# Kernel optimization log

Hardware: AMD Instinct MI355X
Metric: run time of the kernel (lower is better)

## Reference

```python
import jax, jax.numpy as jnp
import numpy as np
import math

B, T, C, H = 8, 1024, 1024, 16
D = C // H  # head_size = 64
FF = 4 * C


def setup_inputs() -> dict:
    key = jax.random.key(0)
    ks = jax.random.split(key, 8)
    s = 0.02
    return {
        "x": jax.random.normal(ks[0], (B, T, C), jnp.float32),
        "ln1_g": jnp.ones((C,), jnp.float32),
        "ln1_b": jnp.zeros((C,), jnp.float32),
        "attn_w": jax.random.normal(ks[1], (C, 3 * C), jnp.float32) * s,
        "attn_b": jnp.zeros((3 * C,), jnp.float32),
        "attn_proj_w": jax.random.normal(ks[2], (C, C), jnp.float32) * s,
        "attn_proj_b": jnp.zeros((C,), jnp.float32),
        "ln2_g": jnp.ones((C,), jnp.float32),
        "ln2_b": jnp.zeros((C,), jnp.float32),
        "fc_w": jax.random.normal(ks[3], (C, FF), jnp.float32) * s,
        "fc_b": jnp.zeros((FF,), jnp.float32),
        "mlp_proj_w": jax.random.normal(ks[4], (FF, C), jnp.float32) * s,
        "mlp_proj_b": jnp.zeros((C,), jnp.float32),
    }


def _layernorm(x, g, b, eps=1e-5):
    mu = jnp.mean(x, axis=-1, keepdims=True)
    var = jnp.mean(jnp.square(x - mu), axis=-1, keepdims=True)
    return (x - mu) * jax.lax.rsqrt(var + eps) * g + b


def reference(x, ln1_g, ln1_b, attn_w, attn_b, attn_proj_w, attn_proj_b,
              ln2_g, ln2_b, fc_w, fc_b, mlp_proj_w, mlp_proj_b):
    # --- attention branch (pre-LN) ---
    h = _layernorm(x, ln1_g, ln1_b)
    kqv = h @ attn_w + attn_b                      # (B,T,3C)
    # NOTE: source splits as k, q, v (k first!)
    k, q, v = jnp.split(kqv, 3, axis=-1)
    k = k.reshape(B, T, H, D).transpose(0, 2, 1, 3)  # (B,H,T,D)
    q = q.reshape(B, T, H, D).transpose(0, 2, 1, 3)
    v = v.reshape(B, T, H, D).transpose(0, 2, 1, 3)
    # NOTE: source computes k @ q^T, i.e. wei[i,j] = k_i . q_j
    scale = 1.0 / math.sqrt(D)
    wei = jnp.einsum('bhid,bhjd->bhij', k, q) * scale  # (B,H,T,T)
    causal = jnp.tril(jnp.ones((T, T), dtype=bool))
    wei = jnp.where(causal, wei, -jnp.inf)
    wei = jax.nn.softmax(wei, axis=-1)
    out = jnp.einsum('bhij,bhjd->bhid', wei, v)        # (B,H,T,D)
    out = out.transpose(0, 2, 1, 3).reshape(B, T, C)
    out = out @ attn_proj_w + attn_proj_b
    x = x + out
    # --- MLP branch (pre-LN) ---
    h2 = _layernorm(x, ln2_g, ln2_b)
    m = jax.nn.gelu(h2 @ fc_w + fc_b, approximate=False)  # torch GELU default = exact erf
    m = m @ mlp_proj_w + mlp_proj_b
    return x + m
```

## Files before the change

kernel.cpp:

```cpp
#include <hip/hip_runtime.h>
#include <stdint.h>

typedef unsigned short u16;
typedef __bf16 bf16x8 __attribute__((ext_vector_type(8)));
typedef float f32x4 __attribute__((ext_vector_type(4)));

#define DEVINL static __device__ __forceinline__

DEVINL u16 f2bf(float f) {
  uint32_t u = __builtin_bit_cast(uint32_t, f);
  u += 0x7fffu + ((u >> 16) & 1u);
  return (u16)(u >> 16);
}

DEVINL uint32_t pack_bf2(float f0, float f1) {
  uint32_t u0 = __builtin_bit_cast(uint32_t, f0) + 0x8000u;
  uint32_t u1 = __builtin_bit_cast(uint32_t, f1) + 0x8000u;
  return __builtin_amdgcn_perm(u1, u0, 0x07060302u);
}

DEVINL bf16x8 ld_frag(const u16* p) { return *(const bf16x8*)p; }

DEVINL void gld_lds16(const void* g, void* l) {
  __builtin_amdgcn_global_load_lds((const __attribute__((address_space(1))) void*)g,
                                   (__attribute__((address_space(3))) void*)l, 16, 0, 0);
}

DEVINL int swz4(int r) { return (r & 3) ^ ((r >> 2) & 3); }

DEVINL void xcd_tile(int& tm, int& tn) {
  const int gx = gridDim.x;
  const int flat = blockIdx.x + gx * blockIdx.y;
  const int q = (gx * gridDim.y) >> 3;
  const int wg = (flat & 7) * q + (flat >> 3);
  tn = (wg % gx) * 128;
  tm = (wg / gx) * 128;
}

__global__ __launch_bounds__(256)
void transpose_bf16(const float* __restrict__ W, u16* __restrict__ Wt, int K, int N) {
  __shared__ float tile[32][33];
  const int n0 = blockIdx.x * 32, k0 = blockIdx.y * 32;
  const int tx = threadIdx.x, ty = threadIdx.y;
#pragma unroll
  for (int i = 0; i < 32; i += 8)
    tile[ty + i][tx] = W[(size_t)(k0 + ty + i) * N + n0 + tx];
  __syncthreads();
#pragma unroll
  for (int i = 0; i < 32; i += 8)
    Wt[(size_t)(n0 + ty + i) * K + k0 + tx] = f2bf(tile[tx][ty + i]);
}

__global__ __launch_bounds__(256)
void ln_kernel(const float* __restrict__ x, const float* __restrict__ g,
               const float* __restrict__ b, u16* __restrict__ out) {
  __shared__ float red[8];
  const size_t row = blockIdx.x;
  const int tid = threadIdx.x;
  float4 v = ((const float4*)(x + row * 1024))[tid];
  float s = v.x + v.y + v.z + v.w;
  float s2 = v.x * v.x + v.y * v.y + v.z * v.z + v.w * v.w;
#pragma unroll
  for (int o = 32; o; o >>= 1) { s += __shfl_down(s, o); s2 += __shfl_down(s2, o); }
  const int w = tid >> 6;
  if ((tid & 63) == 0) { red[w * 2] = s; red[w * 2 + 1] = s2; }
  __syncthreads();
  const float S = red[0] + red[2] + red[4] + red[6];
  const float S2 = red[1] + red[3] + red[5] + red[7];
  const float mu = S * (1.f / 1024.f);
  const float var = S2 * (1.f / 1024.f) - mu * mu;
  const float rstd = rsqrtf(var + 1e-5f);
  float4 gv = ((const float4*)g)[tid];
  float4 bv = ((const float4*)b)[tid];
  ushort4 o;
  o.x = f2bf((v.x - mu) * rstd * gv.x + bv.x);
  o.y = f2bf((v.y - mu) * rstd * gv.y + bv.y);
  o.z = f2bf((v.z - mu) * rstd * gv.z + bv.z);
  o.w = f2bf((v.w - mu) * rstd * gv.w + bv.w);
  ((ushort4*)(out + row * 1024))[tid] = o;
}

enum { EPI_KQV = 0, EPI_RESID = 1, EPI_GELU = 2, EPI_ADD = 3 };

template <int EPI>
DEVINL void gemm_epilogue(f32x4 (&acc)[4][4], const float* __restrict__ bias,
                          void* __restrict__ outp, const float* __restrict__ resid,
                          int N, int tm, int tn, int mh, int nh, int q4, int c) {
#pragma unroll
  for (int mt = 0; mt < 4; ++mt) {
#pragma unroll
    for (int nt = 0; nt < 4; ++nt) {
      const int col = tn + nh + nt * 16 + c;
      const float bcol = bias[col];
#pragma unroll
      for (int rg = 0; rg < 4; ++rg) {
        const int row = tm + mh + mt * 16 + q4 * 4 + rg;
        float val = acc[mt][nt][rg] + bcol;
        if constexpr (EPI == EPI_KQV) {
          const int bb = row >> 10, t = row & 1023;
          const int s = col >> 10, rem = col & 1023;
          const int hh = rem >> 6, d = rem & 63;
          if (s == 0) val *= 0.18033688011112042f;
          const size_t base = ((size_t)((bb * 16 + hh) * 3 + s)) << 16;
          const size_t idx = (s == 2) ? base + (size_t)d * 1024 + t : base + (size_t)t * 64 + d;
          ((u16*)outp)[idx] = f2bf(val);
        } else if constexpr (EPI == EPI_RESID) {
          const size_t idx = (size_t)row * 1024 + col;
          ((float*)outp)[idx] = val + resid[idx];
        } else if constexpr (EPI == EPI_GELU) {
          const float x2 = val * val;
          const float t = __builtin_fmaf(x2, -0.102952445f, -2.30221235f);
          const float e = __builtin_amdgcn_exp2f(val * t);
          const float ge = val * __builtin_amdgcn_rcpf(1.0f + e);
          ((u16*)outp)[(size_t)row * N + col] = f2bf(ge);
        } else {
          const size_t idx = (size_t)row * 1024 + col;
          ((float*)outp)[idx] += val;
        }
      }
    }
  }
}

template <int EPI>
DEVINL void gemm_body2(const u16* __restrict__ A, const u16* __restrict__ Bt,
                       const float* __restrict__ bias, void* __restrict__ outp,
                       const float* __restrict__ resid, int M, int N, int K,
                       int tm, int tn) {
  __shared__ alignas(16) u16 sA[2][128 * 32];
  __shared__ alignas(16) u16 sB[2][128 * 32];
  const int tid = threadIdx.x;
  const int w = tid >> 6, l = tid & 63;
  const int q4 = l >> 4, c = l & 15;
  const int mh = (w >> 1) * 64, nh = (w & 1) * 64;
  const int cg8 = (q4 ^ swz4(c)) * 8;

  f32x4 acc[4][4] = {};

  const int srow = l >> 2;
  const int scol = ((l & 3) ^ swz4(srow)) * 8;
  const u16* gA0 = A + (size_t)(tm + (w * 2) * 16 + srow) * K + scol;
  const u16* gA1 = A + (size_t)(tm + (w * 2 + 1) * 16 + srow) * K + scol;
  const u16* gB0 = Bt + (size_t)(tn + (w * 2) * 16 + srow) * K + scol;
  const u16* gB1 = Bt + (size_t)(tn + (w * 2 + 1) * 16 + srow) * K + scol;
  const int cA0 = (w * 2) * 512, cA1 = (w * 2 + 1) * 512;

  const int nIters = K / 32;
#define STAGE2(buf, k0)                         \
  do {                                          \
    gld_lds16(gA0 + (k0), &sA[buf][cA0]);       \
    gld_lds16(gA1 + (k0), &sA[buf][cA1]);       \
    gld_lds16(gB0 + (k0), &sB[buf][cA0]);       \
    gld_lds16(gB1 + (k0), &sB[buf][cA1]);       \
  } while (0)

  STAGE2(0, 0);
  for (int i = 0; i < nIters; ++i) {
    const int cur = i & 1;
    asm volatile("s_waitcnt vmcnt(0)" ::: "memory");
    __syncthreads();
    if (i + 1 < nIters) STAGE2(cur ^ 1, (i + 1) * 32);
    const u16* bA = sA[cur];
    const u16* bB = sB[cur];
    bf16x8 af[4], bfv[4];
#pragma unroll
    for (int mt = 0; mt < 4; ++mt) af[mt] = ld_frag(bA + (mh + mt * 16 + c) * 32 + cg8);
#pragma unroll
    for (int nt = 0; nt < 4; ++nt) bfv[nt] = ld_frag(bB + (nh + nt * 16 + c) * 32 + cg8);
#pragma unroll
    for (int mt = 0; mt < 4; ++mt)
#pragma unroll
      for (int nt = 0; nt < 4; ++nt)
        acc[mt][nt] = __builtin_amdgcn_mfma_f32_16x16x32_bf16(af[mt], bfv[nt], acc[mt][nt], 0, 0, 0);
  }
#undef STAGE2
  gemm_epilogue<EPI>(acc, bias, outp, resid, N, tm, tn, mh, nh, q4, c);
}

template <int EPI>
DEVINL void gemm_body4(const u16* __restrict__ A, const u16* __restrict__ Bt,
                       const float* __restrict__ bias, void* __restrict__ outp,
                       const float* __restrict__ resid, int M, int N, int K,
                       int tm, int tn) {
  __shared__ alignas(16) u16 sA[4][128 * 32];
  __shared__ alignas(16) u16 sB[4][128 * 32];
  const int tid = threadIdx.x;
  const int w = tid >> 6, l = tid & 63;
  const int q4 = l >> 4, c = l & 15;
  const int mh = (w >> 1) * 64, nh = (w & 1) * 64;
  const int cg8 = (q4 ^ swz4(c)) * 8;

  f32x4 acc[4][4] = {};

  const int srow = l >> 2;
  const int scol = ((l & 3) ^ swz4(srow)) * 8;
  const u16* gA0 = A + (size_t)(tm + (w * 2) * 16 + srow) * K + scol;
  const u16* gA1 = A + (size_t)(tm + (w * 2 + 1) * 16 + srow) * K + scol;
  const u16* gB0 = Bt + (size_t)(tn + (w * 2) * 16 + srow) * K + scol;
  const u16* gB1 = Bt + (size_t)(tn + (w * 2 + 1) * 16 + srow) * K + scol;
  const int cA0 = (w * 2) * 512, cA1 = (w * 2 + 1) * 512;

  const int nIters = K / 32;
#define STAGE4(buf, k0)                         \
  do {                                          \
    gld_lds16(gA0 + (k0), &sA[buf][cA0]);       \
    gld_lds16(gA1 + (k0), &sA[buf][cA1]);       \
    gld_lds16(gB0 + (k0), &sB[buf][cA1 - 512]); \
    gld_lds16(gB1 + (k0), &sB[buf][cA1]);       \
  } while (0)

  auto compute = [&](int cur) {
    const u16* bA = sA[cur];
    const u16* bB = sB[cur];
    bf16x8 af[4], bfv[4];
#pragma unroll
    for (int mt = 0; mt < 4; ++mt) af[mt] = ld_frag(bA + (mh + mt * 16 + c) * 32 + cg8);
#pragma unroll
    for (int nt = 0; nt < 4; ++nt) bfv[nt] = ld_frag(bB + (nh + nt * 16 + c) * 32 + cg8);
#pragma unroll
    for (int mt = 0; mt < 4; ++mt)
#pragma unroll
      for (int nt = 0; nt < 4; ++nt)
        acc[mt][nt] = __builtin_amdgcn_mfma_f32_16x16x32_bf16(af[mt], bfv[nt], acc[mt][nt], 0, 0, 0);
  };

  STAGE4(0, 0);
  STAGE4(1, 32);
  STAGE4(2, 64);
  int i = 0;
  for (; i < nIters - 2; ++i) {
    asm volatile("s_waitcnt vmcnt(8)" ::: "memory");
    __builtin_amdgcn_s_barrier();
    asm volatile("" ::: "memory");
    if (i + 3 < nIters) STAGE4((i + 3) & 3, (i + 3) * 32);
    compute(i & 3);
  }
  asm volatile("s_waitcnt vmcnt(4)" ::: "memory");
  __builtin_amdgcn_s_barrier();
  asm volatile("" ::: "memory");
  compute(i & 3);
  ++i;
  asm volatile("s_waitcnt vmcnt(0)" ::: "memory");
  __builtin_amdgcn_s_barrier();
  asm volatile("" ::: "memory");
  compute(i & 3);
#undef STAGE4
  gemm_epilogue<EPI>(acc, bias, outp, resid, N, tm, tn, mh, nh, q4, c);
}

__global__ __launch_bounds__(256)
void gemm_kqv(const u16* __restrict__ A, const u16* __restrict__ Bt,
              const float* __restrict__ bias, u16* __restrict__ outp,
              int M, int N, int K) {
  int tm, tn;
  xcd_tile(tm, tn);
  gemm_body2<EPI_KQV>(A, Bt, bias, outp, nullptr, M, N, K, tm, tn);
}

__global__ __launch_bounds__(256)
void gemm_gelu(const u16* __restrict__ A, const u16* __restrict__ Bt,
               const float* __restrict__ bias, u16* __restrict__ outp,
               int M, int N, int K) {
  int tm, tn;
  xcd_tile(tm, tn);
  gemm_body2<EPI_GELU>(A, Bt, bias, outp, nullptr, M, N, K, tm, tn);
}

__global__ __launch_bounds__(256)
void gemm_resid(const u16* __restrict__ A, const u16* __restrict__ Bt,
                const float* __restrict__ bias, float* __restrict__ outp,
                const float* __restrict__ resid, int M, int N, int K) {
  int tm, tn;
  xcd_tile(tm, tn);
  gemm_body4<EPI_RESID>(A, Bt, bias, outp, resid, M, N, K, tm, tn);
}

__global__ __launch_bounds__(256)
void gemm_add(const u16* __restrict__ A, const u16* __restrict__ Bt,
              const float* __restrict__ bias, float* __restrict__ outp,
              int M, int N, int K) {
  int tm, tn;
  xcd_tile(tm, tn);
  gemm_body4<EPI_ADD>(A, Bt, bias, outp, nullptr, M, N, K, tm, tn);
}

__global__ __launch_bounds__(256)
void attn_kernel(const u16* __restrict__ kqv, u16* __restrict__ outp) {
  constexpr int LS = 72;
  __shared__ alignas(16) u16 sP[64 * LS];
  __shared__ alignas(16) u16 sK[64 * LS];
  __shared__ alignas(16) u16 sV[64 * LS];
  const int bh = blockIdx.x;
  const int it = (int)gridDim.y - 1 - (int)blockIdx.y;
  const int tid = threadIdx.x;
  const int w = tid >> 6, l = tid & 63, q4 = l >> 4, c = l & 15;
  const int il = w * 16 + c;
  const size_t hb = (size_t)bh * 3 * 65536;
  const u16* qbase = kqv + hb;
  const u16* kbase = kqv + hb + 65536;
  const u16* vbase = kqv + hb + 2 * 65536;

  const int sr = tid >> 3, sc = (tid & 7) * 8;
  const int sr2 = sr + 32;
  *(int4*)&sP[sr * LS + sc] = *(const int4*)(qbase + (size_t)(it * 64 + sr) * 64 + sc);
  *(int4*)&sP[sr2 * LS + sc] = *(const int4*)(qbase + (size_t)(it * 64 + sr2) * 64 + sc);

  f32x4 oacc[4] = {};
  float lsum = 0.f;
  bf16x8 bq0, bq1;

  for (int jt = 0; jt <= it; ++jt) {
    if (jt) __syncthreads();
    *(int4*)&sK[sr * LS + sc] = *(const int4*)(kbase + (size_t)(jt * 64 + sr) * 64 + sc);
    *(int4*)&sK[sr2 * LS + sc] = *(const int4*)(kbase + (size_t)(jt * 64 + sr2) * 64 + sc);
    *(int4*)&sV[sr * LS + sc] = *(const int4*)(vbase + (size_t)sr * 1024 + jt * 64 + sc);
    *(int4*)&sV[sr2 * LS + sc] = *(const int4*)(vbase + (size_t)sr2 * 1024 + jt * 64 + sc);
    __syncthreads();
    if (jt == 0) {
      bq0 = ld_frag(sP + il * LS + q4 * 8);
      bq1 = ld_frag(sP + il * LS + 32 + q4 * 8);
    }

    f32x4 st[4] = {};
#pragma unroll
    for (int nt = 0; nt < 4; ++nt) {
      st[nt] = __builtin_amdgcn_mfma_f32_16x16x32_bf16(
          ld_frag(sK + (nt * 16 + c) * LS + q4 * 8), bq0, st[nt], 0, 0, 0);
      st[nt] = __builtin_amdgcn_mfma_f32_16x16x32_bf16(
          ld_frag(sK + (nt * 16 + c) * LS + 32 + q4 * 8), bq1, st[nt], 0, 0, 0);
    }

    const bool diag = (jt == it);
    u16* prow = sP + il * LS;
#pragma unroll
    for (int nt = 0; nt < 4; ++nt) {
      float e0 = __builtin_amdgcn_exp2f(st[nt][0]);
      float e1 = __builtin_amdgcn_exp2f(st[nt][1]);
      float e2 = __builtin_amdgcn_exp2f(st[nt][2]);
      float e3 = __builtin_amdgcn_exp2f(st[nt][3]);
      if (diag) {
        const int jb = nt * 16 + q4 * 4;
        e0 = (jb + 0 > il) ? 0.f : e0;
        e1 = (jb + 1 > il) ? 0.f : e1;
        e2 = (jb + 2 > il) ? 0.f : e2;
        e3 = (jb + 3 > il) ? 0.f : e3;
      }
      lsum += (e0 + e1) + (e2 + e3);
      uint2 pk = {pack_bf2(e0, e1), pack_bf2(e2, e3)};
      *(uint2*)&prow[nt * 16 + q4 * 4] = pk;
    }

    bf16x8 bp0 = ld_frag(sP + il * LS + q4 * 8);
    bf16x8 bp1 = ld_frag(sP + il * LS + 32 + q4 * 8);
#pragma unroll
    for (int dt = 0; dt < 4; ++dt) {
      oacc[dt] = __builtin_amdgcn_mfma_f32_16x16x32_bf16(
          ld_frag(sV + (dt * 16 + c) * LS + q4 * 8), bp0, oacc[dt], 0, 0, 0);
      oacc[dt] = __builtin_amdgcn_mfma_f32_16x16x32_bf16(
          ld_frag(sV + (dt * 16 + c) * LS + 32 + q4 * 8), bp1, oacc[dt], 0, 0, 0);
    }
  }

  lsum += __shfl_xor(lsum, 16);
  lsum += __shfl_xor(lsum, 32);
  const float linv = 1.f / lsum;

  const int b_ = bh >> 4, h_ = bh & 15;
  const int t_ = it * 64 + il;
  u16* orow = outp + ((size_t)(b_ * 1024 + t_)) * 1024 + h_ * 64;
#pragma unroll
  for (int dt = 0; dt < 4; ++dt) {
    uint2 ok = {pack_bf2(oacc[dt][0] * linv, oacc[dt][1] * linv),
                pack_bf2(oacc[dt][2] * linv, oacc[dt][3] * linv)};
    *(uint2*)&orow[dt * 16 + q4 * 4] = ok;
  }
}

extern "C" void kernel_launch(void* const* d_in, const int* in_sizes, int n_in,
                              void* d_out, int out_size, void* d_ws, size_t ws_size,
                              hipStream_t stream) {
  const float* x       = (const float*)d_in[0];
  const float* ln1_g   = (const float*)d_in[1];
  const float* ln1_b   = (const float*)d_in[2];
  const float* attn_w  = (const float*)d_in[3];
  const float* attn_b  = (const float*)d_in[4];
  const float* attn_pw = (const float*)d_in[5];
  const float* attn_pb = (const float*)d_in[6];
  const float* ln2_g   = (const float*)d_in[7];
  const float* ln2_b   = (const float*)d_in[8];
  const float* fc_w    = (const float*)d_in[9];
  const float* fc_b    = (const float*)d_in[10];
  const float* mlp_w   = (const float*)d_in[11];
  const float* mlp_b   = (const float*)d_in[12];
  float* out = (float*)d_out;

  u16* ws = (u16*)d_ws;
  u16* mlpT     = ws;
  u16* attn_wT  = mlpT + 1024 * 4096;
  u16* attn_pwT = attn_wT + 3072 * 1024;
  u16* fcT      = attn_pwT + 1024 * 1024;
  u16* hbuf     = fcT + 4096 * 1024;
  u16* kqv      = hbuf + 8192 * 1024;
  u16* attn_o   = kqv + (size_t)8192 * 3072;
  u16* mbuf     = kqv;

  dim3 tb(32, 8);
  transpose_bf16<<<dim3(96, 32),  tb, 0, stream>>>(attn_w,  attn_wT,  1024, 3072);
  transpose_bf16<<<dim3(32, 32),  tb, 0, stream>>>(attn_pw, attn_pwT, 1024, 1024);
  transpose_bf16<<<dim3(128, 32), tb, 0, stream>>>(fc_w,    fcT,      1024, 4096);
  transpose_bf16<<<dim3(32, 128), tb, 0, stream>>>(mlp_w,   mlpT,     4096, 1024);

  ln_kernel<<<8192, 256, 0, stream>>>(x, ln1_g, ln1_b, hbuf);

  gemm_kqv<<<dim3(24, 64), 256, 0, stream>>>(hbuf, attn_wT, attn_b, kqv, 8192, 3072, 1024);

  attn_kernel<<<dim3(128, 16), 256, 0, stream>>>(kqv, attn_o);

  gemm_resid<<<dim3(8, 64), 256, 0, stream>>>(attn_o, attn_pwT, attn_pb, out, x,
                                              8192, 1024, 1024);

  ln_kernel<<<8192, 256, 0, stream>>>(out, ln2_g, ln2_b, hbuf);

  gemm_gelu<<<dim3(32, 64), 256, 0, stream>>>(hbuf, fcT, fc_b, mbuf, 8192, 4096, 1024);

  gemm_add<<<dim3(8, 64), 256, 0, stream>>>(mbuf, mlpT, mlp_b, out, 8192, 1024, 4096);
}
```

Measured before the change: 487.2 us.

## Use 256x128 tiles with 512 threads and K=64 stages for N=1024 GEMMs

Replaces the 128x128, 4-stage K=32 GEMM body used by the attention-projection and MLP-down GEMMs with a 512-thread, 256x128 tile body. It uses triple-buffered K=64 LDS stages with XOR swizzle and raises wave priority around the MFMA blocks. A new XCD-aware tile mapping is added for the halved grid. The aim is more reuse of the B operand per block and fewer barriers per K step, at the cost of fewer blocks (256) and larger LDS use per block.

```diff
diff --git a/kernel.cpp b/kernel.cpp
--- a/kernel.cpp
+++ b/kernel.cpp
@@ -178,73 +178,81 @@
 }
 
 template <int EPI>
-DEVINL void gemm_body4(const u16* __restrict__ A, const u16* __restrict__ Bt,
+DEVINL void gemm_bodyW(const u16* __restrict__ A, const u16* __restrict__ Bt,
                        const float* __restrict__ bias, void* __restrict__ outp,
-                       const float* __restrict__ resid, int M, int N, int K,
+                       const float* __restrict__ resid, int N, int K,
                        int tm, int tn) {
-  __shared__ alignas(16) u16 sA[4][128 * 32];
-  __shared__ alignas(16) u16 sB[4][128 * 32];
+  __shared__ alignas(16) u16 sT[3][48 * 512];
   const int tid = threadIdx.x;
   const int w = tid >> 6, l = tid & 63;
   const int q4 = l >> 4, c = l & 15;
   const int mh = (w >> 1) * 64, nh = (w & 1) * 64;
-  const int cg8 = (q4 ^ swz4(c)) * 8;
 
   f32x4 acc[4][4] = {};
 
-  const int srow = l >> 2;
-  const int scol = ((l & 3) ^ swz4(srow)) * 8;
-  const u16* gA0 = A + (size_t)(tm + (w * 2) * 16 + srow) * K + scol;
-  const u16* gA1 = A + (size_t)(tm + (w * 2 + 1) * 16 + srow) * K + scol;
-  const u16* gB0 = Bt + (size_t)(tn + (w * 2) * 16 + srow) * K + scol;
-  const u16* gB1 = Bt + (size_t)(tn + (w * 2 + 1) * 16 + srow) * K + scol;
-  const int cA0 = (w * 2) * 512, cA1 = (w * 2 + 1) * 512;
-
-  const int nIters = K / 32;
-#define STAGE4(buf, k0)                         \
-  do {                                          \
-    gld_lds16(gA0 + (k0), &sA[buf][cA0]);       \
-    gld_lds16(gA1 + (k0), &sA[buf][cA1]);       \
-    gld_lds16(gB0 + (k0), &sB[buf][cA1 - 512]); \
-    gld_lds16(gB1 + (k0), &sB[buf][cA1]);       \
-  } while (0)
-
-  auto compute = [&](int cur) {
-    const u16* bA = sA[cur];
-    const u16* bB = sB[cur];
-    bf16x8 af[4], bfv[4];
-#pragma unroll
-    for (int mt = 0; mt < 4; ++mt) af[mt] = ld_frag(bA + (mh + mt * 16 + c) * 32 + cg8);
-#pragma unroll
-    for (int nt = 0; nt < 4; ++nt) bfv[nt] = ld_frag(bB + (nh + nt * 16 + c) * 32 + cg8);
-#pragma unroll
-    for (int mt = 0; mt < 4; ++mt)
-#pragma unroll
-      for (int nt = 0; nt < 4; ++nt)
-        acc[mt][nt] = __builtin_amdgcn_mfma_f32_16x16x32_bf16(af[mt], bfv[nt], acc[mt][nt], 0, 0, 0);
+  const int lr = l >> 3;
+  const int lc = ((l & 7) ^ lr) * 8;
+  const u16* gA[4];
+  const u16* gB[2];
+#pragma unroll
+  for (int j = 0; j < 4; ++j) gA[j] = A + (size_t)(tm + 32 * w + j * 8 + lr) * K + lc;
+#pragma unroll
+  for (int j = 0; j < 2; ++j) gB[j] = Bt + (size_t)(tn + 16 * w + j * 8 + lr) * K + lc;
+
+  auto stageW = [&](int buf, int k0) {
+#pragma unroll
+    for (int j = 0; j < 4; ++j) gld_lds16(gA[j] + k0, &sT[buf][(4 * w + j) * 512]);
+#pragma unroll
+    for (int j = 0; j < 2; ++j) gld_lds16(gB[j] + k0, &sT[buf][(32 + 2 * w + j) * 512]);
   };
 
-  STAGE4(0, 0);
-  STAGE4(1, 32);
-  STAGE4(2, 64);
+  auto computeW = [&](int cur) {
+    const u16* bufA = sT[cur];
+    const u16* bufB = sT[cur] + 32 * 512;
+#pragma unroll
+    for (int kh = 0; kh < 2; ++kh) {
+      bf16x8 af[4], bfv[4];
+#pragma unroll
+      for (int mt = 0; mt < 4; ++mt) {
+        const int row = mh + mt * 16 + c;
+        af[mt] = ld_frag(bufA + row * 64 + ((kh * 4 + q4) ^ (c & 7)) * 8);
+      }
+#pragma unroll
+      for (int nt = 0; nt < 4; ++nt) {
+        const int row = nh + nt * 16 + c;
+        bfv[nt] = ld_frag(bufB + row * 64 + ((kh * 4 + q4) ^ (c & 7)) * 8);
+      }
+      __builtin_amdgcn_s_setprio(1);
+#pragma unroll
+      for (int mt = 0; mt < 4; ++mt)
+#pragma unroll
+        for (int nt = 0; nt < 4; ++nt)
+          acc[mt][nt] = __builtin_amdgcn_mfma_f32_16x16x32_bf16(af[mt], bfv[nt], acc[mt][nt], 0, 0, 0);
+      __builtin_amdgcn_s_setprio(0);
+    }
+  };
+
+  const int nI = K / 64;
+  stageW(0, 0);
+  stageW(1, 64);
+  int bc = 0;
   int i = 0;
-  for (; i < nIters - 2; ++i) {
-    asm volatile("s_waitcnt vmcnt(8)" ::: "memory");
+  for (; i < nI - 1; ++i) {
+    asm volatile("s_waitcnt vmcnt(6)" ::: "memory");
     __builtin_amdgcn_s_barrier();
     asm volatile("" ::: "memory");
-    if (i + 3 < nIters) STAGE4((i + 3) & 3, (i + 3) * 32);
-    compute(i & 3);
+    if (i + 2 < nI) {
+      const int tgt = (bc >= 1) ? bc - 1 : 2;
+      stageW(tgt, (i + 2) * 64);
+    }
+    computeW(bc);
+    bc = (bc < 2) ? bc + 1 : 0;
   }
-  asm volatile("s_waitcnt vmcnt(4)" ::: "memory");
-  __builtin_amdgcn_s_barrier();
-  asm volatile("" ::: "memory");
-  compute(i & 3);
-  ++i;
   asm volatile("s_waitcnt vmcnt(0)" ::: "memory");
   __builtin_amdgcn_s_barrier();
   asm volatile("" ::: "memory");
-  compute(i & 3);
-#undef STAGE4
+  computeW(bc);
+
   gemm_epilogue<EPI>(acc, bias, outp, resid, N, tm, tn, mh, nh, q4, c);
 }
 
@@ -266,22 +274,29 @@
   gemm_body2<EPI_GELU>(A, Bt, bias, outp, nullptr, M, N, K, tm, tn);
 }
 
-__global__ __launch_bounds__(256)
+DEVINL void xcd_tile_wide(int& tm, int& tn) {
+  const int flat = blockIdx.x + 8 * blockIdx.y;
+  const int wg = (flat & 7) * 32 + (flat >> 3);
+  tn = (wg & 7) * 128;
+  tm = (wg >> 3) * 256;
+}
+
+__global__ __launch_bounds__(512)
 void gemm_resid(const u16* __restrict__ A, const u16* __restrict__ Bt,
                 const float* __restrict__ bias, float* __restrict__ outp,
                 const float* __restrict__ resid, int M, int N, int K) {
   int tm, tn;
-  xcd_tile(tm, tn);
-  gemm_body4<EPI_RESID>(A, Bt, bias, outp, resid, M, N, K, tm, tn);
-}
-
-__global__ __launch_bounds__(256)
+  xcd_tile_wide(tm, tn);
+  gemm_bodyW<EPI_RESID>(A, Bt, bias, outp, resid, N, K, tm, tn);
+}
+
+__global__ __launch_bounds__(512)
 void gemm_add(const u16* __restrict__ A, const u16* __restrict__ Bt,
               const float* __restrict__ bias, float* __restrict__ outp,
               int M, int N, int K) {
   int tm, tn;
-  xcd_tile(tm, tn);
-  gemm_body4<EPI_ADD>(A, Bt, bias, outp, nullptr, M, N, K, tm, tn);
+  xcd_tile_wide(tm, tn);
+  gemm_bodyW<EPI_ADD>(A, Bt, bias, outp, nullptr, N, K, tm, tn);
 }
 
 __global__ __launch_bounds__(256)
@@ -416,12 +431,12 @@
 
   attn_kernel<<<dim3(128, 16), 256, 0, stream>>>(kqv, attn_o);
 
-  gemm_resid<<<dim3(8, 64), 256, 0, stream>>>(attn_o, attn_pwT, attn_pb, out, x,
+  gemm_resid<<<dim3(8, 32), 512, 0, stream>>>(attn_o, attn_pwT, attn_pb, out, x,
                                               8192, 1024, 1024);
 
   ln_kernel<<<8192, 256, 0, stream>>>(out, ln2_g, ln2_b, hbuf);
 
   gemm_gelu<<<dim3(32, 64), 256, 0, stream>>>(hbuf, fcT, fc_b, mbuf, 8192, 4096, 1024);
 
-  gemm_add<<<dim3(8, 64), 256, 0, stream>>>(mbuf, mlpT, mlp_b, out, 8192, 1024, 4096);
-}
+  gemm_add<<<dim3(8, 32), 512, 0, stream>>>(mbuf, mlpT, mlp_b, out, 8192, 1024, 4096);
+}
```

Result: faster. 464.9 us (-4.6%).
